# Kernel tuning notes

Hardware: AMD Instinct MI355X
Metric: run time of the kernel (lower is better)

Reference implementation:

```python
import jax, jax.numpy as jnp
import numpy as np

NUM_HEADS = 12

def setup_inputs() -> dict:
    key = jax.random.key(0)
    k1, k2, k3 = jax.random.split(key, 3)
    B, T, C = 1, 4096, 768
    x = jax.random.normal(k1, (B, T, C), dtype=jnp.float32)
    w_qkv = jax.random.normal(k2, (3 * C, C), dtype=jnp.float32) * (1.0 / np.sqrt(C))
    w_proj = jax.random.normal(k3, (C, C), dtype=jnp.float32) * (1.0 / np.sqrt(C))
    attn_mask = jnp.tril(jnp.ones((T, T), dtype=bool))  # causal block mask
    return {"x": x, "w_qkv": w_qkv, "w_proj": w_proj, "attn_mask": attn_mask}


def reference(x, w_qkv, w_proj, attn_mask):
    B, T, C = x.shape
    H = NUM_HEADS
    Dh = C // H
    # fused QKV projection (torch Linear: y = x @ W.T), then split
    qkv = jnp.einsum('btc,fc->btf', x, w_qkv)  # [B,T,3C]
    q, k, v = jnp.split(qkv, 3, axis=-1)
    # [B,T,C] -> [B,H,T,Dh]
    q = q.reshape(B, T, H, Dh).transpose(0, 2, 1, 3)
    k = k.reshape(B, T, H, Dh).transpose(0, 2, 1, 3)
    v = v.reshape(B, T, H, Dh).transpose(0, 2, 1, 3)
    # masked SDPA, default flex_attention scale = 1/sqrt(head_dim)
    scores = jnp.einsum('bhqd,bhkd->bhqk', q, k) * (1.0 / np.sqrt(Dh))
    neg = jnp.finfo(scores.dtype).min
    scores = jnp.where(attn_mask[None, None, :, :], scores, neg)
    attn = jax.nn.softmax(scores, axis=-1)
    y = jnp.einsum('bhqk,bhkd->bhqd', attn, v)
    # [B,H,T,Dh] -> [B,T,C], then output projection (dropout=0)
    y = y.transpose(0, 2, 1, 3).reshape(B, T, C)
    y = jnp.einsum('btc,fc->btf', y, w_proj)
    return y
```

## Files before the change

kernel.cpp:

```cpp
#include <hip/hip_runtime.h>

typedef unsigned short u16;
typedef unsigned int u32;
typedef __attribute__((ext_vector_type(8))) short s16x8;
typedef __attribute__((ext_vector_type(4))) float f32x4;
typedef __attribute__((ext_vector_type(4))) u16 u16x4;
typedef __attribute__((ext_vector_type(4))) u32 u32x4;

#define LOG2E 1.4426950408889634f

#if __has_builtin(__builtin_amdgcn_exp2f)
#define EXP2F __builtin_amdgcn_exp2f
#else
#define EXP2F exp2f
#endif

__device__ __forceinline__ u16 f32_to_bf16(float f) {
  union { float f; u32 u; } c; c.f = f;
  return (u16)((c.u + 0x7fffu + ((c.u >> 16) & 1u)) >> 16);
}

__device__ __forceinline__ u32 cvtpk(float lo, float hi) {
  u32 r;
  asm("v_cvt_pk_bf16_f32 %0, %1, %2" : "=v"(r) : "v"(lo), "v"(hi));
  return r;
}

__device__ __forceinline__ void async16(const void* g, void* l) {
  __builtin_amdgcn_global_load_lds(
      (__attribute__((address_space(1))) void*)g,
      (__attribute__((address_space(3))) void*)l, 16, 0, 0);
}

__global__ __launch_bounds__(256) void cast3_f32_bf16(const float* __restrict__ a,
                                                      const float* __restrict__ b,
                                                      const float* __restrict__ c,
                                                      u16* __restrict__ out,
                                                      int n1, int n2, int n3) {
  int i = (blockIdx.x * 256 + threadIdx.x) * 4;
  const float* src;
  int off = i;
  if (i < n1) {
    src = a;
  } else if (i < n1 + n2) {
    src = b; off = i - n1;
  } else if (i < n1 + n2 + n3) {
    src = c; off = i - n1 - n2;
  } else {
    return;
  }
  f32x4 v = *(const f32x4*)(src + off);
  u16x4 o;
  o[0] = f32_to_bf16(v[0]);
  o[1] = f32_to_bf16(v[1]);
  o[2] = f32_to_bf16(v[2]);
  o[3] = f32_to_bf16(v[3]);
  *(u16x4*)(out + i) = o;
}

__device__ __forceinline__ int vt_perm_inv(int k) {
  return (k & 35) | ((k & 16) >> 2) | ((k & 12) << 1);
}

__global__ __launch_bounds__(256) void qkv_gemm(const u16* __restrict__ A,
                                                const u16* __restrict__ B,
                                                u16* __restrict__ qk,
                                                u16* __restrict__ vt) {
  constexpr int K = 768;
  constexpr int BK = 32;
  constexpr int NT = K / BK;
  __shared__ alignas(16) u16 As[2][128 * BK];
  __shared__ alignas(16) u16 Bs[2][128 * BK];
  const int tid = threadIdx.x;
  const int lane = tid & 63;
  const int wid = tid >> 6;
  const int brow = blockIdx.x * 128;
  const int bcol = blockIdx.y * 128;
  const int wr = wid >> 1, wc = wid & 1;
  const int l15 = lane & 15, l4 = lane >> 4;
  f32x4 acc[4][4] = {};
  const int c0 = tid, c1 = tid + 256;
  const int r0 = c0 >> 2, s0 = c0 & 3;
  const int r1 = c1 >> 2, s1 = c1 & 3;

#define G1_STAGE(kt, b)                                                        \
  {                                                                            \
    async16(A + (size_t)(brow + r0) * K + (kt) * BK + s0 * 8, &As[b][c0 * 8]); \
    async16(A + (size_t)(brow + r1) * K + (kt) * BK + s1 * 8, &As[b][c1 * 8]); \
    async16(B + (size_t)(bcol + r0) * K + (kt) * BK + s0 * 8, &Bs[b][c0 * 8]); \
    async16(B + (size_t)(bcol + r1) * K + (kt) * BK + s1 * 8, &Bs[b][c1 * 8]); \
  }

  G1_STAGE(0, 0);
  __syncthreads();
  int cur = 0;
  for (int kt = 0; kt < NT; ++kt) {
    if (kt + 1 < NT) G1_STAGE(kt + 1, cur ^ 1);
    s16x8 af[4], bf[4];
#pragma unroll
    for (int m = 0; m < 4; ++m)
      af[m] = *(const s16x8*)&As[cur][(wr * 64 + m * 16 + l15) * BK + l4 * 8];
#pragma unroll
    for (int n = 0; n < 4; ++n)
      bf[n] = *(const s16x8*)&Bs[cur][(wc * 64 + n * 16 + l15) * BK + l4 * 8];
#pragma unroll
    for (int m = 0; m < 4; ++m)
#pragma unroll
      for (int n = 0; n < 4; ++n)
        acc[m][n] = __builtin_amdgcn_mfma_f32_16x16x32_bf16(af[m], bf[n], acc[m][n], 0, 0, 0);
    __syncthreads();
    cur ^= 1;
  }
#undef G1_STAGE

  const int row0 = brow + wr * 64 + l4 * 4;
  const int col0 = bcol + wc * 64 + l15;
  if (bcol >= 1536) {
#pragma unroll
    for (int m = 0; m < 4; ++m) {
      int t0 = row0 + m * 16;
      int s = (t0 & ~63) + vt_perm_inv(t0 & 63);
#pragma unroll
      for (int n = 0; n < 4; ++n) {
        int vcol = col0 + n * 16 - 1536;
        u16x4 pk;
#pragma unroll
        for (int r = 0; r < 4; ++r) pk[r] = f32_to_bf16(acc[m][n][r]);
        *(u16x4*)&vt[(size_t)vcol * 4096 + s] = pk;
      }
    }
  } else {
    const float qs = (bcol < 768) ? 0.125f * LOG2E : 1.0f;
#pragma unroll
    for (int m = 0; m < 4; ++m)
#pragma unroll
      for (int n = 0; n < 4; ++n)
#pragma unroll
        for (int r = 0; r < 4; ++r)
          qk[(size_t)(row0 + m * 16 + r) * 1536 + (col0 + n * 16)] =
              f32_to_bf16(acc[m][n][r] * qs);
  }
}

__global__ __launch_bounds__(256) void proj_gemm(const u16* __restrict__ A,
                                                 const u16* __restrict__ B,
                                                 float* __restrict__ C) {
  constexpr int K = 768;
  constexpr int N = 768;
  constexpr int BK = 32;
  constexpr int NT = K / BK;
  __shared__ alignas(16) u16 As[2][128 * BK];
  __shared__ alignas(16) u16 Bs[2][128 * BK];
  const int tid = threadIdx.x;
  const int lane = tid & 63;
  const int wid = tid >> 6;
  const int brow = blockIdx.x * 128;
  const int bcol = blockIdx.y * 128;
  const int wr = wid >> 1, wc = wid & 1;
  const int l15 = lane & 15, l4 = lane >> 4;
  f32x4 acc[4][4] = {};
  const int c0 = tid, c1 = tid + 256;
  const int r0 = c0 >> 2, s0 = c0 & 3;
  const int r1 = c1 >> 2, s1 = c1 & 3;

#define G2_STAGE(kt, b)                                                        \
  {                                                                            \
    async16(A + (size_t)(brow + r0) * K + (kt) * BK + s0 * 8, &As[b][c0 * 8]); \
    async16(A + (size_t)(brow + r1) * K + (kt) * BK + s1 * 8, &As[b][c1 * 8]); \
    async16(B + (size_t)(bcol + r0) * K + (kt) * BK + s0 * 8, &Bs[b][c0 * 8]); \
    async16(B + (size_t)(bcol + r1) * K + (kt) * BK + s1 * 8, &Bs[b][c1 * 8]); \
  }

  G2_STAGE(0, 0);
  __syncthreads();
  int cur = 0;
  for (int kt = 0; kt < NT; ++kt) {
    if (kt + 1 < NT) G2_STAGE(kt + 1, cur ^ 1);
    s16x8 af[4], bf[4];
#pragma unroll
    for (int m = 0; m < 4; ++m)
      af[m] = *(const s16x8*)&As[cur][(wr * 64 + m * 16 + l15) * BK + l4 * 8];
#pragma unroll
    for (int n = 0; n < 4; ++n)
      bf[n] = *(const s16x8*)&Bs[cur][(wc * 64 + n * 16 + l15) * BK + l4 * 8];
#pragma unroll
    for (int m = 0; m < 4; ++m)
#pragma unroll
      for (int n = 0; n < 4; ++n)
        acc[m][n] = __builtin_amdgcn_mfma_f32_16x16x32_bf16(af[m], bf[n], acc[m][n], 0, 0, 0);
    __syncthreads();
    cur ^= 1;
  }
#undef G2_STAGE

  const int row0 = brow + wr * 64 + l4 * 4;
  const int col0 = bcol + wc * 64 + l15;
#pragma unroll
  for (int m = 0; m < 4; ++m)
#pragma unroll
    for (int n = 0; n < 4; ++n)
#pragma unroll
      for (int r = 0; r < 4; ++r)
        C[(size_t)(row0 + m * 16 + r) * N + (col0 + n * 16)] = acc[m][n][r];
}

constexpr int cph_for(int C) {
  int s = 0;
  for (int qb = 0; qb < 32; ++qb) s += (2 * qb + 2 + C - 1) / C;
  return s;
}

template <int C>
__global__ __launch_bounds__(256) void attn_kernel(const u16* __restrict__ qk,
                                                   const u16* __restrict__ vt,
                                                   u16* __restrict__ y,
                                                   float* __restrict__ po,
                                                   float* __restrict__ pl) {
  constexpr int MAXCH = (64 + C - 1) / C;
  constexpr int CPH = cph_for(C);
  __shared__ alignas(16) u16 Ks[2][64 * 64];
  __shared__ alignas(16) u16 Vs[2][64 * 64];
  const int tid = threadIdx.x;
  const int lane = tid & 63;
  const int wid = tid >> 6;
  const int l15 = lane & 15, l4 = lane >> 4;

  const int h = blockIdx.x % 12;
  int c = CPH - 1 - (int)(blockIdx.x / 12);
  int qb = 0, ch = c;
  for (;;) {
    int n = (2 * qb + 2 + C - 1) / C;
    if (ch < n) break;
    ch -= n;
    ++qb;
  }
  const int NTt = 2 * qb + 2;
  const int nch = (NTt + C - 1) / C;

  const int qw0 = qb * 128 + wid * 32;

  s16x8 bq[2][2];
#pragma unroll
  for (int qf = 0; qf < 2; ++qf)
#pragma unroll
    for (int ks = 0; ks < 2; ++ks)
      bq[qf][ks] = *(const s16x8*)&qk[(size_t)(qw0 + qf * 16 + l15) * 1536 +
                                      h * 64 + ks * 32 + l4 * 8];

  f32x4 o[2][4] = {};
  f32x4 lacc[2] = {};

  const u16* Kb = qk + 768 + h * 64;
  const u16* Vb = vt + (size_t)(h * 64) * 4096;

  const int sc0 = tid, sc1 = tid + 256;
  const int sr0 = sc0 >> 3, sp0 = sc0 & 7;
  const int sr1 = sc1 >> 3, sp1 = sc1 & 7;

#define STAGE_KV(t, b)                                                                        \
  {                                                                                           \
    async16(Kb + (size_t)((t) * 64 + sr0) * 1536 + ((sp0 ^ (sr0 & 7)) * 8), &Ks[b][sc0 * 8]); \
    async16(Kb + (size_t)((t) * 64 + sr1) * 1536 + ((sp1 ^ (sr1 & 7)) * 8), &Ks[b][sc1 * 8]); \
    async16(Vb + (size_t)sr0 * 4096 + (t) * 64 + ((sp0 ^ (sr0 & 7)) * 8), &Vs[b][sc0 * 8]);   \
    async16(Vb + (size_t)sr1 * 4096 + (t) * 64 + ((sp1 ^ (sr1 & 7)) * 8), &Vs[b][sc1 * 8]);   \
  }

  const int t0 = ch * C;
  const int t1 = (t0 + C < NTt) ? t0 + C : NTt;
  STAGE_KV(t0, 0);
  __syncthreads();
  int cur = 0;
  for (int kt = t0; kt < t1; ++kt) {
    if (kt + 1 < t1) STAGE_KV(kt + 1, cur ^ 1);

    f32x4 s4[2][4];
#pragma unroll
    for (int kf = 0; kf < 4; ++kf) {
      int r = kf * 16 + l15;
      s16x8 k0 = *(const s16x8*)&Ks[cur][r * 64 + ((l4 ^ (r & 7)) * 8)];
      s16x8 k1 = *(const s16x8*)&Ks[cur][r * 64 + (((l4 + 4) ^ (r & 7)) * 8)];
#pragma unroll
      for (int qf = 0; qf < 2; ++qf) {
        f32x4 a = {};
        a = __builtin_amdgcn_mfma_f32_16x16x32_bf16(k0, bq[qf][0], a, 0, 0, 0);
        a = __builtin_amdgcn_mfma_f32_16x16x32_bf16(k1, bq[qf][1], a, 0, 0, 0);
        s4[qf][kf] = a;
      }
    }
    if (kt >= 2 * qb) {
#pragma unroll
      for (int qf = 0; qf < 2; ++qf) {
        int qg = qw0 + qf * 16 + l15;
#pragma unroll
        for (int kf = 0; kf < 4; ++kf)
#pragma unroll
          for (int r = 0; r < 4; ++r)
            if (kt * 64 + kf * 16 + l4 * 4 + r > qg) s4[qf][kf][r] = -1e30f;
      }
    }
    u32 w[2][4][2];
#pragma unroll
    for (int qf = 0; qf < 2; ++qf)
#pragma unroll
      for (int kf = 0; kf < 4; ++kf) {
        f32x4 p;
#pragma unroll
        for (int r = 0; r < 4; ++r) p[r] = EXP2F(s4[qf][kf][r]);
        lacc[qf] += p;
        w[qf][kf][0] = cvtpk(p[0], p[1]);
        w[qf][kf][1] = cvtpk(p[2], p[3]);
      }
#pragma unroll
    for (int ks2 = 0; ks2 < 2; ++ks2) {
      s16x8 bp[2];
#pragma unroll
      for (int qf = 0; qf < 2; ++qf) {
        u32x4 bu;
        bu[0] = w[qf][2 * ks2][0];
        bu[1] = w[qf][2 * ks2][1];
        bu[2] = w[qf][2 * ks2 + 1][0];
        bu[3] = w[qf][2 * ks2 + 1][1];
        bp[qf] = __builtin_bit_cast(s16x8, bu);
      }
#pragma unroll
      for (int df = 0; df < 4; ++df) {
        int d = df * 16 + l15;
        int e = ks2 * 4 + l4;
        s16x8 av = *(const s16x8*)&Vs[cur][d * 64 + ((e ^ (d & 7)) * 8)];
#pragma unroll
        for (int qf = 0; qf < 2; ++qf)
          o[qf][df] = __builtin_amdgcn_mfma_f32_16x16x32_bf16(av, bp[qf], o[qf][df], 0, 0, 0);
      }
    }
    __syncthreads();
    cur ^= 1;
  }
#undef STAGE_KV

  float lsum[2];
#pragma unroll
  for (int qf = 0; qf < 2; ++qf) {
    float s = lacc[qf][0] + lacc[qf][1] + lacc[qf][2] + lacc[qf][3];
    s += __shfl_xor(s, 16);
    s += __shfl_xor(s, 32);
    lsum[qf] = s;
  }

  if (nch == 1) {
#pragma unroll
    for (int qf = 0; qf < 2; ++qf) {
      float inv = 1.0f / lsum[qf];
#pragma unroll
      for (int df = 0; df < 4; ++df) {
        u16x4 pk;
#pragma unroll
        for (int r = 0; r < 4; ++r) pk[r] = f32_to_bf16(o[qf][df][r] * inv);
        *(u16x4*)&y[(size_t)(qw0 + qf * 16 + l15) * 768 + h * 64 + df * 16 + l4 * 4] = pk;
      }
    }
  } else {
    const size_t slot = (size_t)(h * 32 + qb) * MAXCH + ch;
#pragma unroll
    for (int qf = 0; qf < 2; ++qf) {
      float* ob = po + slot * 8192 + (size_t)(wid * 32 + qf * 16 + l15) * 64;
#pragma unroll
      for (int df = 0; df < 4; ++df)
        *(f32x4*)(ob + df * 16 + l4 * 4) = o[qf][df];
      if (lane < 16) pl[slot * 128 + wid * 32 + qf * 16 + l15] = lsum[qf];
    }
  }
}

template <int C>
__global__ __launch_bounds__(256) void attn_combine(const float* __restrict__ po,
                                                    const float* __restrict__ pl,
                                                    u16* __restrict__ y) {
  constexpr int MAXCH = (64 + C - 1) / C;
  const int h = blockIdx.x;
  const int qb = C / 2 + blockIdx.y;
  const int nch = (2 * qb + 2 + C - 1) / C;
  const int tid = threadIdx.x;
  const int q = tid >> 1;
  const int d0 = (tid & 1) * 32;

  f32x4 acc[8] = {};
  float lt = 0.f;
  for (int s = 0; s < nch; ++s) {
    const size_t slot = (size_t)(h * 32 + qb) * MAXCH + s;
    lt += pl[slot * 128 + q];
    const float* ob = po + slot * 8192 + (size_t)q * 64 + d0;
#pragma unroll
    for (int j = 0; j < 8; ++j) acc[j] += *(const f32x4*)(ob + j * 4);
  }
  float inv = 1.0f / lt;
  u16* yp = &y[(size_t)(qb * 128 + q) * 768 + h * 64 + d0];
#pragma unroll
  for (int j = 0; j < 8; ++j) {
    u16x4 pk;
#pragma unroll
    for (int r = 0; r < 4; ++r) pk[r] = f32_to_bf16(acc[j][r] * inv);
    *(u16x4*)(yp + j * 4) = pk;
  }
}

extern "C" void kernel_launch(void* const* d_in, const int* in_sizes, int n_in,
                              void* d_out, int out_size, void* d_ws, size_t ws_size,
                              hipStream_t stream) {
  const float* x = (const float*)d_in[0];
  const float* w_qkv = (const float*)d_in[1];
  const float* w_proj = (const float*)d_in[2];
  float* out = (float*)d_out;

  u16* ws = (u16*)d_ws;
  u16* xb = ws;
  u16* wqkvb = xb + 4096 * 768;
  u16* wprojb = wqkvb + 2304 * 768;
  u16* qkb = wprojb + 768 * 768;
  u16* vtb = qkb + (size_t)4096 * 1536;
  u16* yb = vtb + (size_t)768 * 4096;
  const size_t base_u16 = (size_t)4096 * 768 + 2304 * 768 + 768 * 768 +
                          (size_t)4096 * 1536 + (size_t)768 * 4096 + (size_t)4096 * 768;
  float* pf = (float*)(ws + base_u16);
  const size_t base_b = base_u16 * 2;

  constexpr int N1 = 4096 * 768, N2 = 2304 * 768, N3 = 768 * 768;
  cast3_f32_bf16<<<(N1 + N2 + N3) / 4 / 256, 256, 0, stream>>>(
      x, w_qkv, w_proj, xb, N1, N2, N3);

  qkv_gemm<<<dim3(32, 18), 256, 0, stream>>>(xb, wqkvb, qkb, vtb);

  const size_t need16 = base_b + (size_t)(12 * 32 * 4) * (8192 + 128) * 4;
  const size_t need32 = base_b + (size_t)(12 * 32 * 2) * (8192 + 128) * 4;
  if (ws_size >= need16) {
    constexpr int C = 16, MAXCH = 4;
    float* po = pf;
    float* pl = po + (size_t)12 * 32 * MAXCH * 8192;
    attn_kernel<C><<<12 * cph_for(C), 256, 0, stream>>>(qkb, vtb, yb, po, pl);
    attn_combine<C><<<dim3(12, 32 - C / 2), 256, 0, stream>>>(po, pl, yb);
  } else if (ws_size >= need32) {
    constexpr int C = 32, MAXCH = 2;
    float* po = pf;
    float* pl = po + (size_t)12 * 32 * MAXCH * 8192;
    attn_kernel<C><<<12 * cph_for(C), 256, 0, stream>>>(qkb, vtb, yb, po, pl);
    attn_combine<C><<<dim3(12, 32 - C / 2), 256, 0, stream>>>(po, pl, yb);
  } else {
    constexpr int C = 64;
    attn_kernel<C><<<12 * cph_for(C), 256, 0, stream>>>(qkb, vtb, yb, nullptr, nullptr);
  }

  proj_gemm<<<dim3(32, 6), 256, 0, stream>>>(yb, wprojb, out);
}
```

Baseline: 119.5 us.

## Use 512-thread GEMM blocks, add setprio around attention MFMAs, finer KV split

```diff
diff --git a/kernel.cpp b/kernel.cpp
--- a/kernel.cpp
+++ b/kernel.cpp
@@ -62,7 +62,7 @@
   return (k & 35) | ((k & 16) >> 2) | ((k & 12) << 1);
 }
 
-__global__ __launch_bounds__(256) void qkv_gemm(const u16* __restrict__ A,
+__global__ __launch_bounds__(512) void qkv_gemm(const u16* __restrict__ A,
                                                 const u16* __restrict__ B,
                                                 u16* __restrict__ qk,
                                                 u16* __restrict__ vt) {
@@ -76,19 +76,15 @@
   const int wid = tid >> 6;
   const int brow = blockIdx.x * 128;
   const int bcol = blockIdx.y * 128;
-  const int wr = wid >> 1, wc = wid & 1;
+  const int wr = wid >> 2, wc = wid & 3;
   const int l15 = lane & 15, l4 = lane >> 4;
-  f32x4 acc[4][4] = {};
-  const int c0 = tid, c1 = tid + 256;
-  const int r0 = c0 >> 2, s0 = c0 & 3;
-  const int r1 = c1 >> 2, s1 = c1 & 3;
-
-#define G1_STAGE(kt, b)                                                        \
-  {                                                                            \
-    async16(A + (size_t)(brow + r0) * K + (kt) * BK + s0 * 8, &As[b][c0 * 8]); \
-    async16(A + (size_t)(brow + r1) * K + (kt) * BK + s1 * 8, &As[b][c1 * 8]); \
-    async16(B + (size_t)(bcol + r0) * K + (kt) * BK + s0 * 8, &Bs[b][c0 * 8]); \
-    async16(B + (size_t)(bcol + r1) * K + (kt) * BK + s1 * 8, &Bs[b][c1 * 8]); \
+  f32x4 acc[4][2] = {};
+  const int r0 = tid >> 2, s0 = tid & 3;
+
+#define G1_STAGE(kt, b)                                                         \
+  {                                                                             \
+    async16(A + (size_t)(brow + r0) * K + (kt) * BK + s0 * 8, &As[b][tid * 8]); \
+    async16(B + (size_t)(bcol + r0) * K + (kt) * BK + s0 * 8, &Bs[b][tid * 8]); \
   }
 
   G1_STAGE(0, 0);
@@ -96,17 +92,17 @@
   int cur = 0;
   for (int kt = 0; kt < NT; ++kt) {
     if (kt + 1 < NT) G1_STAGE(kt + 1, cur ^ 1);
-    s16x8 af[4], bf[4];
+    s16x8 af[4], bf[2];
 #pragma unroll
     for (int m = 0; m < 4; ++m)
       af[m] = *(const s16x8*)&As[cur][(wr * 64 + m * 16 + l15) * BK + l4 * 8];
 #pragma unroll
-    for (int n = 0; n < 4; ++n)
-      bf[n] = *(const s16x8*)&Bs[cur][(wc * 64 + n * 16 + l15) * BK + l4 * 8];
+    for (int n = 0; n < 2; ++n)
+      bf[n] = *(const s16x8*)&Bs[cur][(wc * 32 + n * 16 + l15) * BK + l4 * 8];
 #pragma unroll
     for (int m = 0; m < 4; ++m)
 #pragma unroll
-      for (int n = 0; n < 4; ++n)
+      for (int n = 0; n < 2; ++n)
         acc[m][n] = __builtin_amdgcn_mfma_f32_16x16x32_bf16(af[m], bf[n], acc[m][n], 0, 0, 0);
     __syncthreads();
     cur ^= 1;
@@ -114,14 +110,14 @@
 #undef G1_STAGE
 
   const int row0 = brow + wr * 64 + l4 * 4;
-  const int col0 = bcol + wc * 64 + l15;
+  const int col0 = bcol + wc * 32 + l15;
   if (bcol >= 1536) {
 #pragma unroll
     for (int m = 0; m < 4; ++m) {
       int t0 = row0 + m * 16;
       int s = (t0 & ~63) + vt_perm_inv(t0 & 63);
 #pragma unroll
-      for (int n = 0; n < 4; ++n) {
+      for (int n = 0; n < 2; ++n) {
         int vcol = col0 + n * 16 - 1536;
         u16x4 pk;
 #pragma unroll
@@ -134,7 +130,7 @@
 #pragma unroll
     for (int m = 0; m < 4; ++m)
 #pragma unroll
-      for (int n = 0; n < 4; ++n)
+      for (int n = 0; n < 2; ++n)
 #pragma unroll
         for (int r = 0; r < 4; ++r)
           qk[(size_t)(row0 + m * 16 + r) * 1536 + (col0 + n * 16)] =
@@ -142,7 +138,7 @@
   }
 }
 
-__global__ __launch_bounds__(256) void proj_gemm(const u16* __restrict__ A,
+__global__ __launch_bounds__(512) void proj_gemm(const u16* __restrict__ A,
                                                  const u16* __restrict__ B,
                                                  float* __restrict__ C) {
   constexpr int K = 768;
@@ -156,19 +152,15 @@
   const int wid = tid >> 6;
   const int brow = blockIdx.x * 128;
   const int bcol = blockIdx.y * 128;
-  const int wr = wid >> 1, wc = wid & 1;
+  const int wr = wid >> 2, wc = wid & 3;
   const int l15 = lane & 15, l4 = lane >> 4;
-  f32x4 acc[4][4] = {};
-  const int c0 = tid, c1 = tid + 256;
-  const int r0 = c0 >> 2, s0 = c0 & 3;
-  const int r1 = c1 >> 2, s1 = c1 & 3;
-
-#define G2_STAGE(kt, b)                                                        \
-  {                                                                            \
-    async16(A + (size_t)(brow + r0) * K + (kt) * BK + s0 * 8, &As[b][c0 * 8]); \
-    async16(A + (size_t)(brow + r1) * K + (kt) * BK + s1 * 8, &As[b][c1 * 8]); \
-    async16(B + (size_t)(bcol + r0) * K + (kt) * BK + s0 * 8, &Bs[b][c0 * 8]); \
-    async16(B + (size_t)(bcol + r1) * K + (kt) * BK + s1 * 8, &Bs[b][c1 * 8]); \
+  f32x4 acc[4][2] = {};
+  const int r0 = tid >> 2, s0 = tid & 3;
+
+#define G2_STAGE(kt, b)                                                         \
+  {                                                                             \
+    async16(A + (size_t)(brow + r0) * K + (kt) * BK + s0 * 8, &As[b][tid * 8]); \
+    async16(B + (size_t)(bcol + r0) * K + (kt) * BK + s0 * 8, &Bs[b][tid * 8]); \
   }
 
   G2_STAGE(0, 0);
@@ -176,17 +168,17 @@
   int cur = 0;
   for (int kt = 0; kt < NT; ++kt) {
     if (kt + 1 < NT) G2_STAGE(kt + 1, cur ^ 1);
-    s16x8 af[4], bf[4];
+    s16x8 af[4], bf[2];
 #pragma unroll
     for (int m = 0; m < 4; ++m)
       af[m] = *(const s16x8*)&As[cur][(wr * 64 + m * 16 + l15) * BK + l4 * 8];
 #pragma unroll
-    for (int n = 0; n < 4; ++n)
-      bf[n] = *(const s16x8*)&Bs[cur][(wc * 64 + n * 16 + l15) * BK + l4 * 8];
+    for (int n = 0; n < 2; ++n)
+      bf[n] = *(const s16x8*)&Bs[cur][(wc * 32 + n * 16 + l15) * BK + l4 * 8];
 #pragma unroll
     for (int m = 0; m < 4; ++m)
 #pragma unroll
-      for (int n = 0; n < 4; ++n)
+      for (int n = 0; n < 2; ++n)
         acc[m][n] = __builtin_amdgcn_mfma_f32_16x16x32_bf16(af[m], bf[n], acc[m][n], 0, 0, 0);
     __syncthreads();
     cur ^= 1;
@@ -194,11 +186,11 @@
 #undef G2_STAGE
 
   const int row0 = brow + wr * 64 + l4 * 4;
-  const int col0 = bcol + wc * 64 + l15;
+  const int col0 = bcol + wc * 32 + l15;
 #pragma unroll
   for (int m = 0; m < 4; ++m)
 #pragma unroll
-    for (int n = 0; n < 4; ++n)
+    for (int n = 0; n < 2; ++n)
 #pragma unroll
       for (int r = 0; r < 4; ++r)
         C[(size_t)(row0 + m * 16 + r) * N + (col0 + n * 16)] = acc[m][n][r];
@@ -274,6 +266,7 @@
     if (kt + 1 < t1) STAGE_KV(kt + 1, cur ^ 1);
 
     f32x4 s4[2][4];
+    __builtin_amdgcn_s_setprio(1);
 #pragma unroll
     for (int kf = 0; kf < 4; ++kf) {
       int r = kf * 16 + l15;
@@ -287,6 +280,7 @@
         s4[qf][kf] = a;
       }
     }
+    __builtin_amdgcn_s_setprio(0);
     if (kt >= 2 * qb) {
 #pragma unroll
       for (int qf = 0; qf < 2; ++qf) {
@@ -310,6 +304,7 @@
         w[qf][kf][0] = cvtpk(p[0], p[1]);
         w[qf][kf][1] = cvtpk(p[2], p[3]);
       }
+    __builtin_amdgcn_s_setprio(1);
 #pragma unroll
     for (int ks2 = 0; ks2 < 2; ++ks2) {
       s16x8 bp[2];
@@ -332,6 +327,7 @@
           o[qf][df] = __builtin_amdgcn_mfma_f32_16x16x32_bf16(av, bp[qf], o[qf][df], 0, 0, 0);
       }
     }
+    __builtin_amdgcn_s_setprio(0);
     __syncthreads();
     cur ^= 1;
   }
@@ -427,11 +423,18 @@
   cast3_f32_bf16<<<(N1 + N2 + N3) / 4 / 256, 256, 0, stream>>>(
       x, w_qkv, w_proj, xb, N1, N2, N3);
 
-  qkv_gemm<<<dim3(32, 18), 256, 0, stream>>>(xb, wqkvb, qkb, vtb);
-
+  qkv_gemm<<<dim3(32, 18), 512, 0, stream>>>(xb, wqkvb, qkb, vtb);
+
+  const size_t need8 = base_b + (size_t)(12 * 32 * 8) * (8192 + 128) * 4;
   const size_t need16 = base_b + (size_t)(12 * 32 * 4) * (8192 + 128) * 4;
   const size_t need32 = base_b + (size_t)(12 * 32 * 2) * (8192 + 128) * 4;
-  if (ws_size >= need16) {
+  if (ws_size >= need8) {
+    constexpr int C = 8, MAXCH = 8;
+    float* po = pf;
+    float* pl = po + (size_t)12 * 32 * MAXCH * 8192;
+    attn_kernel<C><<<12 * cph_for(C), 256, 0, stream>>>(qkb, vtb, yb, po, pl);
+    attn_combine<C><<<dim3(12, 32 - C / 2), 256, 0, stream>>>(po, pl, yb);
+  } else if (ws_size >= need16) {
     constexpr int C = 16, MAXCH = 4;
     float* po = pf;
     float* pl = po + (size_t)12 * 32 * MAXCH * 8192;
@@ -448,5 +451,5 @@
     attn_kernel<C><<<12 * cph_for(C), 256, 0, stream>>>(qkb, vtb, yb, nullptr, nullptr);
   }
 
-  proj_gemm<<<dim3(32, 6), 256, 0, stream>>>(yb, wprojb, out);
-}
+  proj_gemm<<<dim3(32, 6), 512, 0, stream>>>(yb, wprojb, out);
+}
```

Result: faster. 114.3 us (-4.4%).
